# Optimization experiments

Measured on AMD Instinct MI355X. Metric: run time of the kernel, lower is better.

Reference implementation:

```python
import jax, jax.numpy as jnp
import numpy as np

N = 4096
IN_DIM, HID, OUT_DIM = 512, 256, 128
GAMMA = 6.0            # MCP weight truncation: w(y) = max(1 - y/gamma, 0)
LAM_HAT = 0.9
LAM = 1.0 / LAM_HAT - 1.0
PROP_STEPS = 10


def setup_inputs() -> dict:
    key = jax.random.key(0)
    k_a, k_f, k_w1, k_b1, k_w2, k_b2 = jax.random.split(key, 6)
    p = 32.0 / N  # avg degree ~32
    U = jax.random.uniform(k_a, (N, N))
    A = (U < p).astype(jnp.float32)
    A = jnp.maximum(A, A.T)                       # symmetric
    A = A * (1.0 - jnp.eye(N, dtype=jnp.float32))  # zero diagonal (loops added in forward)
    F = jax.random.normal(k_f, (N, IN_DIM), dtype=jnp.float32)
    W1 = jax.random.normal(k_w1, (IN_DIM, HID), dtype=jnp.float32) * 0.05
    b1 = jax.random.normal(k_b1, (HID,), dtype=jnp.float32) * 0.01
    W2 = jax.random.normal(k_w2, (HID, OUT_DIM), dtype=jnp.float32) * 0.05
    b2 = jax.random.normal(k_b2, (OUT_DIM,), dtype=jnp.float32) * 0.01
    return {"A": A, "F": F, "W1": W1, "b1": b1, "W2": W2, "b2": b2}


def reference(A, F, W1, b1, W2, b2):
    n = A.shape[0]
    # MLP (eval mode: dropout off)
    F0 = jnp.maximum(F @ W1 + b1, 0.0) @ W2 + b2          # [N, out_dim]
    # add self loops
    A = A + jnp.eye(n, dtype=A.dtype)
    D = A.sum(-1)                                          # [N]
    D_sq = jnp.sqrt(D)[:, None]                            # [N,1]
    A_t = A / (D_sq * D_sq.T)                              # sym-normalized adjacency
    diag = jnp.arange(n)
    Fc = F0
    for _ in range(PROP_STEPS):
        X = Fc / D_sq                                      # [N, d]
        sq = jnp.sum(X * X, axis=-1)                       # [N]
        Z = sq[:, None] + sq[None, :] - 2.0 * (X @ X.T)    # pairwise squared dist [N,N]
        Z = jax.lax.stop_gradient(jnp.maximum(Z, 0.0))
        Wm = jnp.maximum(1.0 - jnp.sqrt(Z) / GAMMA, 0.0)   # MCP IRLS weight
        Wm = Wm.at[diag, diag].set(0.0)
        Wm = jnp.where(jnp.isnan(Wm), 1.0, Wm)
        # quasi-Newton IRLS step
        Q = ((Wm * A).sum(-1) / D + LAM)[:, None]          # [N,1]
        Fc = (Wm * A_t) @ Fc / Q + LAM * F0 / Q
    return Fc
```

## Files before the change

kernel.cpp:

```cpp
#include <hip/hip_runtime.h>

#define NN 4096
#define IN_DIM 512
#define HID 256
#define OUT_DIM 128
#define MAXDEG 192
#define INV_GAMMA (1.0f / 6.0f)
#define LAM 0.11111111111111116f
#define PROP_STEPS 10

__global__ void k_analyze(const float* __restrict__ A, unsigned short* __restrict__ cols,
                          int* __restrict__ deg, float* __restrict__ DsqInv,
                          float* __restrict__ Dinv) {
    int wid = threadIdx.x >> 6, lane = threadIdx.x & 63;
    int row = blockIdx.x * 4 + wid;
    const float4* Ar = (const float4*)(A + (size_t)row * NN);
    unsigned short* crow = cols + (size_t)row * MAXDEG;
    int cnt = 0;
    float fsum = 0.f;
    for (int it = 0; it < NN / 256; ++it) {
        float4 v = Ar[it * 64 + lane];
        fsum += (v.x + v.y) + (v.z + v.w);
        int colbase = (it * 64 + lane) * 4;
        float comp[4] = {v.x, v.y, v.z, v.w};
#pragma unroll
        for (int c = 0; c < 4; ++c) {
            bool nz = (comp[c] != 0.f);
            unsigned long long m = __ballot(nz);
            if (nz) {
                int off = cnt + __popcll(m & ((1ull << lane) - 1ull));
                if (off < MAXDEG) crow[off] = (unsigned short)(colbase + c);
            }
            cnt += __popcll(m);
        }
    }
#pragma unroll
    for (int m = 1; m < 64; m <<= 1) fsum += __shfl_xor(fsum, m);
    if (lane == 0) {
        float D = fsum + 1.0f;
        deg[row] = cnt < MAXDEG ? cnt : MAXDEG;
        DsqInv[row] = 1.0f / sqrtf(D);
        Dinv[row] = 1.0f / D;
    }
}

__global__ __launch_bounds__(256) void k_mlp(const float* __restrict__ F,
                      const float* __restrict__ W1, const float* __restrict__ b1,
                      const float* __restrict__ W2, const float* __restrict__ b2,
                      const float* __restrict__ DsqInv,
                      float* __restrict__ F0, float* __restrict__ X0) {
    __shared__ __align__(16) float sF[8 * IN_DIM];
    __shared__ __align__(16) float sW[32 * 256];
    __shared__ __align__(16) float sH[8 * HID];
    int r0 = blockIdx.x * 8;
    int t = threadIdx.x;
#pragma unroll
    for (int i = 0; i < 4; ++i) {
        int idx = i * 256 + t;
        int r = idx >> 7, q = idx & 127;
        *(float4*)&sF[r * IN_DIM + 4 * q] = *(const float4*)&F[(size_t)(r0 + r) * IN_DIM + 4 * q];
    }
    {
        int cq = t & 63, rg = t >> 6;
        float4 accA = make_float4(0.f, 0.f, 0.f, 0.f);
        float4 accB = make_float4(0.f, 0.f, 0.f, 0.f);
        for (int kt = 0; kt < IN_DIM / 32; ++kt) {
            __syncthreads();
#pragma unroll
            for (int i = 0; i < 8; ++i) {
                int idx = i * 256 + t;
                int kr = idx >> 6, q = idx & 63;
                *(float4*)&sW[kr * 256 + 4 * q] =
                    *(const float4*)&W1[(size_t)(kt * 32 + kr) * HID + 4 * q];
            }
            __syncthreads();
#pragma unroll
            for (int kk = 0; kk < 32; ++kk) {
                int k = kt * 32 + kk;
                float4 w = *(float4*)&sW[kk * 256 + 4 * cq];
                float fa = sF[(2 * rg) * IN_DIM + k];
                float fb = sF[(2 * rg + 1) * IN_DIM + k];
                accA.x = fmaf(fa, w.x, accA.x); accA.y = fmaf(fa, w.y, accA.y);
                accA.z = fmaf(fa, w.z, accA.z); accA.w = fmaf(fa, w.w, accA.w);
                accB.x = fmaf(fb, w.x, accB.x); accB.y = fmaf(fb, w.y, accB.y);
                accB.z = fmaf(fb, w.z, accB.z); accB.w = fmaf(fb, w.w, accB.w);
            }
        }
        float4 b = *(const float4*)&b1[4 * cq];
        float4 ha, hb;
        ha.x = fmaxf(accA.x + b.x, 0.f); ha.y = fmaxf(accA.y + b.y, 0.f);
        ha.z = fmaxf(accA.z + b.z, 0.f); ha.w = fmaxf(accA.w + b.w, 0.f);
        hb.x = fmaxf(accB.x + b.x, 0.f); hb.y = fmaxf(accB.y + b.y, 0.f);
        hb.z = fmaxf(accB.z + b.z, 0.f); hb.w = fmaxf(accB.w + b.w, 0.f);
        *(float4*)&sH[(2 * rg) * HID + 4 * cq] = ha;
        *(float4*)&sH[(2 * rg + 1) * HID + 4 * cq] = hb;
    }
    {
        int c = t & 127, half = t >> 7;
        float acc2[4] = {0.f, 0.f, 0.f, 0.f};
        for (int kt = 0; kt < HID / 32; ++kt) {
            __syncthreads();
#pragma unroll
            for (int i = 0; i < 4; ++i) {
                int idx = i * 256 + t;
                int kr = idx >> 5, q = idx & 31;
                *(float4*)&sW[kr * 128 + 4 * q] =
                    *(const float4*)&W2[(size_t)(kt * 32 + kr) * OUT_DIM + 4 * q];
            }
            __syncthreads();
#pragma unroll
            for (int kk = 0; kk < 32; ++kk) {
                int k = kt * 32 + kk;
                float w = sW[kk * 128 + c];
#pragma unroll
                for (int r = 0; r < 4; ++r)
                    acc2[r] = fmaf(sH[(half * 4 + r) * HID + k], w, acc2[r]);
            }
        }
        float b = b2[c];
#pragma unroll
        for (int r = 0; r < 4; ++r) {
            int row = r0 + half * 4 + r;
            float v = acc2[r] + b;
            F0[(size_t)row * OUT_DIM + c] = v;
            X0[(size_t)row * OUT_DIM + c] = v * DsqInv[row];
        }
    }
}

__global__ __launch_bounds__(256) void k_prop(const float* __restrict__ X,
                       const float* __restrict__ F0,
                       const unsigned short* __restrict__ cols, const int* __restrict__ deg,
                       const float* __restrict__ DsqInv, const float* __restrict__ Dinv,
                       float* __restrict__ Xout, float* __restrict__ FcOut, int final_step) {
    __shared__ unsigned short sCols[4][MAXDEG];
    int wid = threadIdx.x >> 6, lane = threadIdx.x & 63;
    int row = blockIdx.x * 4 + wid;
    int g = lane >> 3, oc = lane & 7;
    int dg = deg[row];
    float dsi = DsqInv[row], di = Dinv[row];
    for (int e = lane; e < dg; e += 64) sCols[wid][e] = cols[(size_t)row * MAXDEG + e];
    const float4* Xi4 = (const float4*)(X + (size_t)row * 128 + oc * 16);
    float4 xi0 = Xi4[0], xi1 = Xi4[1], xi2 = Xi4[2], xi3 = Xi4[3];
    float sqi;
    {
        float s = 0.f;
        s = fmaf(xi0.x, xi0.x, s); s = fmaf(xi0.y, xi0.y, s);
        s = fmaf(xi0.z, xi0.z, s); s = fmaf(xi0.w, xi0.w, s);
        s = fmaf(xi1.x, xi1.x, s); s = fmaf(xi1.y, xi1.y, s);
        s = fmaf(xi1.z, xi1.z, s); s = fmaf(xi1.w, xi1.w, s);
        s = fmaf(xi2.x, xi2.x, s); s = fmaf(xi2.y, xi2.y, s);
        s = fmaf(xi2.z, xi2.z, s); s = fmaf(xi2.w, xi2.w, s);
        s = fmaf(xi3.x, xi3.x, s); s = fmaf(xi3.y, xi3.y, s);
        s = fmaf(xi3.z, xi3.z, s); s = fmaf(xi3.w, xi3.w, s);
        s += __shfl_xor(s, 1); s += __shfl_xor(s, 2); s += __shfl_xor(s, 4);
        sqi = s;
    }
    float acc[16];
#pragma unroll
    for (int i = 0; i < 16; ++i) acc[i] = 0.f;
    float qacc = 0.f;
    int nch = (dg + 7) >> 3;
    for (int ch = 0; ch < nch; ++ch) {
        int e = ch * 8 + g;
        bool act = (e < dg);
        int ec = act ? e : (dg - 1);
        int j = (int)sCols[wid][ec];
        const float4* Xj4 = (const float4*)(X + (size_t)j * 128 + oc * 16);
        float4 a = Xj4[0], b = Xj4[1], c = Xj4[2], d = Xj4[3];
        float p = 0.f, sj = 0.f;
        p = fmaf(xi0.x, a.x, p); sj = fmaf(a.x, a.x, sj);
        p = fmaf(xi0.y, a.y, p); sj = fmaf(a.y, a.y, sj);
        p = fmaf(xi0.z, a.z, p); sj = fmaf(a.z, a.z, sj);
        p = fmaf(xi0.w, a.w, p); sj = fmaf(a.w, a.w, sj);
        p = fmaf(xi1.x, b.x, p); sj = fmaf(b.x, b.x, sj);
        p = fmaf(xi1.y, b.y, p); sj = fmaf(b.y, b.y, sj);
        p = fmaf(xi1.z, b.z, p); sj = fmaf(b.z, b.z, sj);
        p = fmaf(xi1.w, b.w, p); sj = fmaf(b.w, b.w, sj);
        p = fmaf(xi2.x, c.x, p); sj = fmaf(c.x, c.x, sj);
        p = fmaf(xi2.y, c.y, p); sj = fmaf(c.y, c.y, sj);
        p = fmaf(xi2.z, c.z, p); sj = fmaf(c.z, c.z, sj);
        p = fmaf(xi2.w, c.w, p); sj = fmaf(c.w, c.w, sj);
        p = fmaf(xi3.x, d.x, p); sj = fmaf(d.x, d.x, sj);
        p = fmaf(xi3.y, d.y, p); sj = fmaf(d.y, d.y, sj);
        p = fmaf(xi3.z, d.z, p); sj = fmaf(d.z, d.z, sj);
        p = fmaf(xi3.w, d.w, p); sj = fmaf(d.w, d.w, sj);
        p += __shfl_xor(p, 1); p += __shfl_xor(p, 2); p += __shfl_xor(p, 4);
        sj += __shfl_xor(sj, 1); sj += __shfl_xor(sj, 2); sj += __shfl_xor(sj, 4);
        float z = fmaxf(sqi + sj - 2.f * p, 0.f);
        float w = fmaxf(1.f - sqrtf(z) * INV_GAMMA, 0.f);
        w = act ? w : 0.f;
        qacc += w;
        acc[0]  = fmaf(w, a.x, acc[0]);  acc[1]  = fmaf(w, a.y, acc[1]);
        acc[2]  = fmaf(w, a.z, acc[2]);  acc[3]  = fmaf(w, a.w, acc[3]);
        acc[4]  = fmaf(w, b.x, acc[4]);  acc[5]  = fmaf(w, b.y, acc[5]);
        acc[6]  = fmaf(w, b.z, acc[6]);  acc[7]  = fmaf(w, b.w, acc[7]);
        acc[8]  = fmaf(w, c.x, acc[8]);  acc[9]  = fmaf(w, c.y, acc[9]);
        acc[10] = fmaf(w, c.z, acc[10]); acc[11] = fmaf(w, c.w, acc[11]);
        acc[12] = fmaf(w, d.x, acc[12]); acc[13] = fmaf(w, d.y, acc[13]);
        acc[14] = fmaf(w, d.z, acc[14]); acc[15] = fmaf(w, d.w, acc[15]);
    }
#pragma unroll
    for (int m = 8; m <= 32; m <<= 1) {
        qacc += __shfl_xor(qacc, m);
#pragma unroll
        for (int i = 0; i < 16; ++i) acc[i] += __shfl_xor(acc[i], m);
    }
    float invQ = 1.f / (qacc * di + LAM);
    if (g == 0) {
        const float4* F04 = (const float4*)(F0 + (size_t)row * 128 + oc * 16);
        float* dstF = (float*)(FcOut + (size_t)row * 128 + oc * 16);
        float* dstX = (float*)(Xout + (size_t)row * 128 + oc * 16);
#pragma unroll
        for (int q = 0; q < 4; ++q) {
            float4 f0 = F04[q];
            float4 o;
            o.x = (dsi * acc[4 * q + 0] + LAM * f0.x) * invQ;
            o.y = (dsi * acc[4 * q + 1] + LAM * f0.y) * invQ;
            o.z = (dsi * acc[4 * q + 2] + LAM * f0.z) * invQ;
            o.w = (dsi * acc[4 * q + 3] + LAM * f0.w) * invQ;
            if (final_step) {
                *(float4*)&dstF[4 * q] = o;
            } else {
                float4 xo;
                xo.x = o.x * dsi; xo.y = o.y * dsi; xo.z = o.z * dsi; xo.w = o.w * dsi;
                *(float4*)&dstX[4 * q] = xo;
            }
        }
    }
}

extern "C" void kernel_launch(void* const* d_in, const int* in_sizes, int n_in,
                              void* d_out, int out_size, void* d_ws, size_t ws_size,
                              hipStream_t stream) {
    const float *A = nullptr, *F = nullptr, *W1 = nullptr, *b1 = nullptr,
                *W2 = nullptr, *b2 = nullptr;
    for (int i = 0; i < n_in; i++) {
        switch (in_sizes[i]) {
            case NN * NN:        A  = (const float*)d_in[i]; break;
            case NN * IN_DIM:    F  = (const float*)d_in[i]; break;
            case IN_DIM * HID:   W1 = (const float*)d_in[i]; break;
            case HID:            b1 = (const float*)d_in[i]; break;
            case HID * OUT_DIM:  W2 = (const float*)d_in[i]; break;
            case OUT_DIM:        b2 = (const float*)d_in[i]; break;
            default: break;
        }
    }
    float* out = (float*)d_out;

    char* ws = (char*)d_ws;
    float* F0     = (float*)ws; ws += (size_t)NN * OUT_DIM * 4;
    float* XA     = (float*)ws; ws += (size_t)NN * OUT_DIM * 4;
    float* XB     = (float*)ws; ws += (size_t)NN * OUT_DIM * 4;
    float* DsqInv = (float*)ws; ws += (size_t)NN * 4;
    float* Dinv   = (float*)ws; ws += (size_t)NN * 4;
    int*   deg    = (int*)ws;   ws += (size_t)NN * 4;
    unsigned short* cols = (unsigned short*)ws; ws += (size_t)NN * MAXDEG * 2;

    hipLaunchKernelGGL(k_analyze, dim3(NN / 4), dim3(256), 0, stream, A, cols, deg, DsqInv, Dinv);
    hipLaunchKernelGGL(k_mlp, dim3(NN / 8), dim3(256), 0, stream,
                       F, W1, b1, W2, b2, DsqInv, F0, XA);

    float* Xc = XA; float* Xn = XB;
    for (int step = 0; step < PROP_STEPS; step++) {
        int fin = (step == PROP_STEPS - 1) ? 1 : 0;
        hipLaunchKernelGGL(k_prop, dim3(NN / 4), dim3(256), 0, stream,
                           Xc, F0, cols, deg, DsqInv, Dinv, Xn, out, fin);
        float* t1 = Xc; Xc = Xn; Xn = t1;
    }
}
```

Baseline: 289.8 us.

## Precompute row norms and split each row's neighbor loop across two waves

```diff
diff --git a/kernel.cpp b/kernel.cpp
--- a/kernel.cpp
+++ b/kernel.cpp
@@ -54,11 +54,13 @@
     __shared__ __align__(16) float sH[8 * HID];
     int r0 = blockIdx.x * 8;
     int t = threadIdx.x;
+    float4* sF4 = (float4*)sF;
+    float4* sW4 = (float4*)sW;
 #pragma unroll
     for (int i = 0; i < 4; ++i) {
         int idx = i * 256 + t;
         int r = idx >> 7, q = idx & 127;
-        *(float4*)&sF[r * IN_DIM + 4 * q] = *(const float4*)&F[(size_t)(r0 + r) * IN_DIM + 4 * q];
+        sF4[r * 128 + q] = *(const float4*)&F[(size_t)(r0 + r) * IN_DIM + 4 * q];
     }
     {
         int cq = t & 63, rg = t >> 6;
@@ -70,20 +72,33 @@
             for (int i = 0; i < 8; ++i) {
                 int idx = i * 256 + t;
                 int kr = idx >> 6, q = idx & 63;
-                *(float4*)&sW[kr * 256 + 4 * q] =
-                    *(const float4*)&W1[(size_t)(kt * 32 + kr) * HID + 4 * q];
-            }
-            __syncthreads();
-#pragma unroll
-            for (int kk = 0; kk < 32; ++kk) {
-                int k = kt * 32 + kk;
-                float4 w = *(float4*)&sW[kk * 256 + 4 * cq];
-                float fa = sF[(2 * rg) * IN_DIM + k];
-                float fb = sF[(2 * rg + 1) * IN_DIM + k];
-                accA.x = fmaf(fa, w.x, accA.x); accA.y = fmaf(fa, w.y, accA.y);
-                accA.z = fmaf(fa, w.z, accA.z); accA.w = fmaf(fa, w.w, accA.w);
-                accB.x = fmaf(fb, w.x, accB.x); accB.y = fmaf(fb, w.y, accB.y);
-                accB.z = fmaf(fb, w.z, accB.z); accB.w = fmaf(fb, w.w, accB.w);
+                sW4[kr * 64 + q] = *(const float4*)&W1[(size_t)(kt * 32 + kr) * HID + 4 * q];
+            }
+            __syncthreads();
+#pragma unroll
+            for (int g4 = 0; g4 < 8; ++g4) {
+                float4 w0 = sW4[(4 * g4 + 0) * 64 + cq];
+                float4 w1 = sW4[(4 * g4 + 1) * 64 + cq];
+                float4 w2 = sW4[(4 * g4 + 2) * 64 + cq];
+                float4 w3 = sW4[(4 * g4 + 3) * 64 + cq];
+                float4 fA = sF4[(2 * rg) * 128 + kt * 8 + g4];
+                float4 fB = sF4[(2 * rg + 1) * 128 + kt * 8 + g4];
+                accA.x = fmaf(fA.x, w0.x, accA.x); accA.y = fmaf(fA.x, w0.y, accA.y);
+                accA.z = fmaf(fA.x, w0.z, accA.z); accA.w = fmaf(fA.x, w0.w, accA.w);
+                accA.x = fmaf(fA.y, w1.x, accA.x); accA.y = fmaf(fA.y, w1.y, accA.y);
+                accA.z = fmaf(fA.y, w1.z, accA.z); accA.w = fmaf(fA.y, w1.w, accA.w);
+                accA.x = fmaf(fA.z, w2.x, accA.x); accA.y = fmaf(fA.z, w2.y, accA.y);
+                accA.z = fmaf(fA.z, w2.z, accA.z); accA.w = fmaf(fA.z, w2.w, accA.w);
+                accA.x = fmaf(fA.w, w3.x, accA.x); accA.y = fmaf(fA.w, w3.y, accA.y);
+                accA.z = fmaf(fA.w, w3.z, accA.z); accA.w = fmaf(fA.w, w3.w, accA.w);
+                accB.x = fmaf(fB.x, w0.x, accB.x); accB.y = fmaf(fB.x, w0.y, accB.y);
+                accB.z = fmaf(fB.x, w0.z, accB.z); accB.w = fmaf(fB.x, w0.w, accB.w);
+                accB.x = fmaf(fB.y, w1.x, accB.x); accB.y = fmaf(fB.y, w1.y, accB.y);
+                accB.z = fmaf(fB.y, w1.z, accB.z); accB.w = fmaf(fB.y, w1.w, accB.w);
+                accB.x = fmaf(fB.z, w2.x, accB.x); accB.y = fmaf(fB.z, w2.y, accB.y);
+                accB.z = fmaf(fB.z, w2.z, accB.z); accB.w = fmaf(fB.z, w2.w, accB.w);
+                accB.x = fmaf(fB.w, w3.x, accB.x); accB.y = fmaf(fB.w, w3.y, accB.y);
+                accB.z = fmaf(fB.w, w3.z, accB.z); accB.w = fmaf(fB.w, w3.w, accB.w);
             }
         }
         float4 b = *(const float4*)&b1[4 * cq];
@@ -104,8 +119,7 @@
             for (int i = 0; i < 4; ++i) {
                 int idx = i * 256 + t;
                 int kr = idx >> 5, q = idx & 31;
-                *(float4*)&sW[kr * 128 + 4 * q] =
-                    *(const float4*)&W2[(size_t)(kt * 32 + kr) * OUT_DIM + 4 * q];
+                sW4[kr * 32 + q] = *(const float4*)&W2[(size_t)(kt * 32 + kr) * OUT_DIM + 4 * q];
             }
             __syncthreads();
 #pragma unroll
@@ -128,106 +142,108 @@
     }
 }
 
-__global__ __launch_bounds__(256) void k_prop(const float* __restrict__ X,
+__global__ void k_sq0(const float* __restrict__ X, float* __restrict__ sq) {
+    int wid = threadIdx.x >> 6, lane = threadIdx.x & 63;
+    int row = blockIdx.x * 4 + wid;
+    float2 x = ((const float2*)X)[row * 64 + lane];
+    float s = x.x * x.x + x.y * x.y;
+#pragma unroll
+    for (int m = 1; m < 64; m <<= 1) s += __shfl_xor(s, m);
+    if (lane == 0) sq[row] = s;
+}
+
+__global__ __launch_bounds__(256, 6) void k_prop(const float* __restrict__ X,
                        const float* __restrict__ F0,
                        const unsigned short* __restrict__ cols, const int* __restrict__ deg,
                        const float* __restrict__ DsqInv, const float* __restrict__ Dinv,
-                       float* __restrict__ Xout, float* __restrict__ FcOut, int final_step) {
-    __shared__ unsigned short sCols[4][MAXDEG];
-    int wid = threadIdx.x >> 6, lane = threadIdx.x & 63;
-    int row = blockIdx.x * 4 + wid;
+                       const float* __restrict__ sq_in,
+                       float* __restrict__ Xout, float* __restrict__ sq_out,
+                       float* __restrict__ FcOut, int final_step) {
+    __shared__ unsigned short sCols[2][MAXDEG];
+    __shared__ float sPart[2][16][130];
+    __shared__ float sQw[2][2];
+    int t = threadIdx.x;
+    int wave = t >> 6, lane = t & 63;
+    int rl = wave >> 1, half = wave & 1;
+    int row = blockIdx.x * 2 + rl;
     int g = lane >> 3, oc = lane & 7;
     int dg = deg[row];
-    float dsi = DsqInv[row], di = Dinv[row];
-    for (int e = lane; e < dg; e += 64) sCols[wid][e] = cols[(size_t)row * MAXDEG + e];
+    {
+        int idx = half * 64 + lane;
+        for (int e = idx; e < dg; e += 128)
+            sCols[rl][e] = cols[(size_t)row * MAXDEG + e];
+    }
+    float sqi = sq_in[row];
     const float4* Xi4 = (const float4*)(X + (size_t)row * 128 + oc * 16);
     float4 xi0 = Xi4[0], xi1 = Xi4[1], xi2 = Xi4[2], xi3 = Xi4[3];
-    float sqi;
-    {
-        float s = 0.f;
-        s = fmaf(xi0.x, xi0.x, s); s = fmaf(xi0.y, xi0.y, s);
-        s = fmaf(xi0.z, xi0.z, s); s = fmaf(xi0.w, xi0.w, s);
-        s = fmaf(xi1.x, xi1.x, s); s = fmaf(xi1.y, xi1.y, s);
-        s = fmaf(xi1.z, xi1.z, s); s = fmaf(xi1.w, xi1.w, s);
-        s = fmaf(xi2.x, xi2.x, s); s = fmaf(xi2.y, xi2.y, s);
-        s = fmaf(xi2.z, xi2.z, s); s = fmaf(xi2.w, xi2.w, s);
-        s = fmaf(xi3.x, xi3.x, s); s = fmaf(xi3.y, xi3.y, s);
-        s = fmaf(xi3.z, xi3.z, s); s = fmaf(xi3.w, xi3.w, s);
-        s += __shfl_xor(s, 1); s += __shfl_xor(s, 2); s += __shfl_xor(s, 4);
-        sqi = s;
-    }
-    float acc[16];
-#pragma unroll
-    for (int i = 0; i < 16; ++i) acc[i] = 0.f;
+    __syncthreads();
+    float4 a0 = make_float4(0.f,0.f,0.f,0.f), a1 = make_float4(0.f,0.f,0.f,0.f);
+    float4 a2 = make_float4(0.f,0.f,0.f,0.f), a3 = make_float4(0.f,0.f,0.f,0.f);
     float qacc = 0.f;
-    int nch = (dg + 7) >> 3;
+    int nch = (dg + 15) >> 4;
     for (int ch = 0; ch < nch; ++ch) {
-        int e = ch * 8 + g;
-        bool act = (e < dg);
-        int ec = act ? e : (dg - 1);
-        int j = (int)sCols[wid][ec];
+        int e = ch * 16 + half * 8 + g;
+        bool act = e < dg;
+        int j = (int)sCols[rl][act ? e : 0];
         const float4* Xj4 = (const float4*)(X + (size_t)j * 128 + oc * 16);
-        float4 a = Xj4[0], b = Xj4[1], c = Xj4[2], d = Xj4[3];
-        float p = 0.f, sj = 0.f;
-        p = fmaf(xi0.x, a.x, p); sj = fmaf(a.x, a.x, sj);
-        p = fmaf(xi0.y, a.y, p); sj = fmaf(a.y, a.y, sj);
-        p = fmaf(xi0.z, a.z, p); sj = fmaf(a.z, a.z, sj);
-        p = fmaf(xi0.w, a.w, p); sj = fmaf(a.w, a.w, sj);
-        p = fmaf(xi1.x, b.x, p); sj = fmaf(b.x, b.x, sj);
-        p = fmaf(xi1.y, b.y, p); sj = fmaf(b.y, b.y, sj);
-        p = fmaf(xi1.z, b.z, p); sj = fmaf(b.z, b.z, sj);
-        p = fmaf(xi1.w, b.w, p); sj = fmaf(b.w, b.w, sj);
-        p = fmaf(xi2.x, c.x, p); sj = fmaf(c.x, c.x, sj);
-        p = fmaf(xi2.y, c.y, p); sj = fmaf(c.y, c.y, sj);
-        p = fmaf(xi2.z, c.z, p); sj = fmaf(c.z, c.z, sj);
-        p = fmaf(xi2.w, c.w, p); sj = fmaf(c.w, c.w, sj);
-        p = fmaf(xi3.x, d.x, p); sj = fmaf(d.x, d.x, sj);
-        p = fmaf(xi3.y, d.y, p); sj = fmaf(d.y, d.y, sj);
-        p = fmaf(xi3.z, d.z, p); sj = fmaf(d.z, d.z, sj);
-        p = fmaf(xi3.w, d.w, p); sj = fmaf(d.w, d.w, sj);
-        p += __shfl_xor(p, 1); p += __shfl_xor(p, 2); p += __shfl_xor(p, 4);
-        sj += __shfl_xor(sj, 1); sj += __shfl_xor(sj, 2); sj += __shfl_xor(sj, 4);
-        float z = fmaxf(sqi + sj - 2.f * p, 0.f);
+        float4 c0 = Xj4[0], c1 = Xj4[1], c2 = Xj4[2], c3 = Xj4[3];
+        float sqj = sq_in[j];
+        float pA = 0.f, pB = 0.f;
+        pA = fmaf(xi0.x, c0.x, pA); pB = fmaf(xi0.y, c0.y, pB);
+        pA = fmaf(xi0.z, c0.z, pA); pB = fmaf(xi0.w, c0.w, pB);
+        pA = fmaf(xi1.x, c1.x, pA); pB = fmaf(xi1.y, c1.y, pB);
+        pA = fmaf(xi1.z, c1.z, pA); pB = fmaf(xi1.w, c1.w, pB);
+        pA = fmaf(xi2.x, c2.x, pA); pB = fmaf(xi2.y, c2.y, pB);
+        pA = fmaf(xi2.z, c2.z, pA); pB = fmaf(xi2.w, c2.w, pB);
+        pA = fmaf(xi3.x, c3.x, pA); pB = fmaf(xi3.y, c3.y, pB);
+        pA = fmaf(xi3.z, c3.z, pA); pB = fmaf(xi3.w, c3.w, pB);
+        float p = pA + pB;
+        p += __shfl_xor(p, 1);
+        p += __shfl_xor(p, 2);
+        p += __shfl_xor(p, 4);
+        float z = fmaxf(sqi + sqj - 2.f * p, 0.f);
         float w = fmaxf(1.f - sqrtf(z) * INV_GAMMA, 0.f);
         w = act ? w : 0.f;
         qacc += w;
-        acc[0]  = fmaf(w, a.x, acc[0]);  acc[1]  = fmaf(w, a.y, acc[1]);
-        acc[2]  = fmaf(w, a.z, acc[2]);  acc[3]  = fmaf(w, a.w, acc[3]);
-        acc[4]  = fmaf(w, b.x, acc[4]);  acc[5]  = fmaf(w, b.y, acc[5]);
-        acc[6]  = fmaf(w, b.z, acc[6]);  acc[7]  = fmaf(w, b.w, acc[7]);
-        acc[8]  = fmaf(w, c.x, acc[8]);  acc[9]  = fmaf(w, c.y, acc[9]);
-        acc[10] = fmaf(w, c.z, acc[10]); acc[11] = fmaf(w, c.w, acc[11]);
-        acc[12] = fmaf(w, d.x, acc[12]); acc[13] = fmaf(w, d.y, acc[13]);
-        acc[14] = fmaf(w, d.z, acc[14]); acc[15] = fmaf(w, d.w, acc[15]);
-    }
-#pragma unroll
-    for (int m = 8; m <= 32; m <<= 1) {
-        qacc += __shfl_xor(qacc, m);
-#pragma unroll
-        for (int i = 0; i < 16; ++i) acc[i] += __shfl_xor(acc[i], m);
-    }
-    float invQ = 1.f / (qacc * di + LAM);
-    if (g == 0) {
-        const float4* F04 = (const float4*)(F0 + (size_t)row * 128 + oc * 16);
-        float* dstF = (float*)(FcOut + (size_t)row * 128 + oc * 16);
-        float* dstX = (float*)(Xout + (size_t)row * 128 + oc * 16);
-#pragma unroll
-        for (int q = 0; q < 4; ++q) {
-            float4 f0 = F04[q];
-            float4 o;
-            o.x = (dsi * acc[4 * q + 0] + LAM * f0.x) * invQ;
-            o.y = (dsi * acc[4 * q + 1] + LAM * f0.y) * invQ;
-            o.z = (dsi * acc[4 * q + 2] + LAM * f0.z) * invQ;
-            o.w = (dsi * acc[4 * q + 3] + LAM * f0.w) * invQ;
-            if (final_step) {
-                *(float4*)&dstF[4 * q] = o;
-            } else {
-                float4 xo;
-                xo.x = o.x * dsi; xo.y = o.y * dsi; xo.z = o.z * dsi; xo.w = o.w * dsi;
-                *(float4*)&dstX[4 * q] = xo;
-            }
-        }
-    }
+        a0.x = fmaf(w, c0.x, a0.x); a0.y = fmaf(w, c0.y, a0.y);
+        a0.z = fmaf(w, c0.z, a0.z); a0.w = fmaf(w, c0.w, a0.w);
+        a1.x = fmaf(w, c1.x, a1.x); a1.y = fmaf(w, c1.y, a1.y);
+        a1.z = fmaf(w, c1.z, a1.z); a1.w = fmaf(w, c1.w, a1.w);
+        a2.x = fmaf(w, c2.x, a2.x); a2.y = fmaf(w, c2.y, a2.y);
+        a2.z = fmaf(w, c2.z, a2.z); a2.w = fmaf(w, c2.w, a2.w);
+        a3.x = fmaf(w, c3.x, a3.x); a3.y = fmaf(w, c3.y, a3.y);
+        a3.z = fmaf(w, c3.z, a3.z); a3.w = fmaf(w, c3.w, a3.w);
+    }
+    int slot = half * 8 + g;
+    *(float4*)&sPart[rl][slot][oc * 16 + 0]  = a0;
+    *(float4*)&sPart[rl][slot][oc * 16 + 4]  = a1;
+    *(float4*)&sPart[rl][slot][oc * 16 + 8]  = a2;
+    *(float4*)&sPart[rl][slot][oc * 16 + 12] = a3;
+    if (oc == 0) sPart[rl][slot][128] = qacc;
+    __syncthreads();
+    int rl2 = t >> 7, d = t & 127;
+    int row2 = blockIdx.x * 2 + rl2;
+    float acc = 0.f, qs = 0.f;
+#pragma unroll
+    for (int s = 0; s < 16; ++s) {
+        acc += sPart[rl2][s][d];
+        qs  += sPart[rl2][s][128];
+    }
+    float dsi = DsqInv[row2];
+    float invQ = 1.f / (qs * Dinv[row2] + LAM);
+    float o = (dsi * acc + LAM * F0[(size_t)row2 * 128 + d]) * invQ;
+    if (final_step) {
+        FcOut[(size_t)row2 * 128 + d] = o;
+    } else {
+        float x = o * dsi;
+        Xout[(size_t)row2 * 128 + d] = x;
+        float ss = x * x;
+#pragma unroll
+        for (int m = 1; m < 64; m <<= 1) ss += __shfl_xor(ss, m);
+        if (lane == 0) sQw[rl2][wave & 1] = ss;
+    }
+    __syncthreads();
+    if (!final_step && t < 2) sq_out[blockIdx.x * 2 + t] = sQw[t][0] + sQw[t][1];
 }
 
 extern "C" void kernel_launch(void* const* d_in, const int* in_sizes, int n_in,
@@ -254,18 +270,23 @@
     float* XB     = (float*)ws; ws += (size_t)NN * OUT_DIM * 4;
     float* DsqInv = (float*)ws; ws += (size_t)NN * 4;
     float* Dinv   = (float*)ws; ws += (size_t)NN * 4;
+    float* sqA    = (float*)ws; ws += (size_t)NN * 4;
+    float* sqB    = (float*)ws; ws += (size_t)NN * 4;
     int*   deg    = (int*)ws;   ws += (size_t)NN * 4;
     unsigned short* cols = (unsigned short*)ws; ws += (size_t)NN * MAXDEG * 2;
 
     hipLaunchKernelGGL(k_analyze, dim3(NN / 4), dim3(256), 0, stream, A, cols, deg, DsqInv, Dinv);
     hipLaunchKernelGGL(k_mlp, dim3(NN / 8), dim3(256), 0, stream,
                        F, W1, b1, W2, b2, DsqInv, F0, XA);
+    hipLaunchKernelGGL(k_sq0, dim3(NN / 4), dim3(256), 0, stream, XA, sqA);
 
     float* Xc = XA; float* Xn = XB;
+    float* sqc = sqA; float* sqn = sqB;
     for (int step = 0; step < PROP_STEPS; step++) {
         int fin = (step == PROP_STEPS - 1) ? 1 : 0;
-        hipLaunchKernelGGL(k_prop, dim3(NN / 4), dim3(256), 0, stream,
-                           Xc, F0, cols, deg, DsqInv, Dinv, Xn, out, fin);
+        hipLaunchKernelGGL(k_prop, dim3(NN / 2), dim3(256), 0, stream,
+                           Xc, F0, cols, deg, DsqInv, Dinv, sqc, Xn, sqn, out, fin);
         float* t1 = Xc; Xc = Xn; Xn = t1;
-    }
-}
+        float* t2 = sqc; sqc = sqn; sqn = t2;
+    }
+}
```

Measured after the change: 318.8 us. 10.0% more time.
